# Kernel optimization log

Hardware: AMD Instinct MI355X
Metric: run time of the kernel (lower is better)

## Reference

```python
import jax, jax.numpy as jnp
import numpy as np
import math

N_HEADS = 16
ROPE_BASE = 10000.0


def rotate_half(x):
    x1 = x[..., ::2]
    x2 = x[..., 1::2]
    return jnp.stack((-x2, x1), axis=-1).reshape(x.shape)


def rope_tables(seq_len, head_dim, dtype):
    inv_freq = 1.0 / (ROPE_BASE ** (jnp.arange(0, head_dim, 2, dtype=jnp.float32) / head_dim))
    positions = jnp.arange(seq_len, dtype=jnp.float32)
    freqs = jnp.outer(positions, inv_freq)            # [S, hd/2]
    emb = jnp.concatenate((freqs, freqs), axis=-1)    # [S, hd]  (matches torch cat convention)
    cos = jnp.cos(emb)[None, None, :, :].astype(dtype)
    sin = jnp.sin(emb)[None, None, :, :].astype(dtype)
    return cos, sin


def setup_inputs() -> dict:
    key = jax.random.key(0)
    k1, k2, k3 = jax.random.split(key, 3)
    B, S, D = 2, 2048, 1024
    x = jax.random.normal(k1, (B, S, D), dtype=jnp.float32)
    # causal lower-triangular mask, broadcastable over batch and heads
    mask = jnp.tril(jnp.ones((S, S), dtype=jnp.int32))[None, None, :, :]
    w_qkv = jax.random.normal(k2, (D, 3 * D), dtype=jnp.float32) * 0.02
    w_out = jax.random.normal(k3, (D, D), dtype=jnp.float32) * 0.02
    return {"x": x, "mask": mask, "w_qkv": w_qkv, "w_out": w_out}


def reference(x, mask, w_qkv, w_out):
    B, S, D = x.shape
    H = N_HEADS
    hd = D // H
    qkv = (x @ w_qkv).reshape(B, S, 3, H, hd)
    qkv = jnp.transpose(qkv, (2, 0, 3, 1, 4))         # [3, B, H, S, hd]
    q, k, v = qkv[0], qkv[1], qkv[2]
    cos, sin = rope_tables(S, hd, x.dtype)
    q = q * cos + rotate_half(q) * sin
    k = k * cos + rotate_half(k) * sin
    scale = math.sqrt(hd)
    attn = jnp.einsum("bhsd,bhtd->bhst", q, k) / scale
    attn = jnp.where(mask == 0, -jnp.inf, attn)
    attn = jax.nn.softmax(attn, axis=-1)              # dropout p=0.0 -> identity
    out = jnp.einsum("bhst,bhtd->bhsd", attn, v)
    out = jnp.transpose(out, (0, 2, 1, 3)).reshape(B, S, D)
    return out @ w_out
```

## Files before the change

### kernel.cpp

```cpp
#include <hip/hip_runtime.h>
#include <stdint.h>

typedef unsigned short u16;
typedef __bf16 bf16x8 __attribute__((ext_vector_type(8)));
typedef float f32x4 __attribute__((ext_vector_type(4)));

#define S_LEN 2048
#define NH    16
#define DM    1024
#define N3    3072
#define MROWS 4096

__device__ __forceinline__ float b2f(u16 u) {
  unsigned int v = ((unsigned int)u) << 16;
  return __builtin_bit_cast(float, v);
}
__device__ __forceinline__ u16 f2b(float f) {
  unsigned int v = __builtin_bit_cast(unsigned int, f);
  v += 0x7fffu + ((v >> 16) & 1u);
  return (u16)(v >> 16);
}
__device__ __forceinline__ u16 f2b_trunc(float f) {
  return (u16)(__builtin_bit_cast(unsigned int, f) >> 16);
}
__device__ __forceinline__ bf16x8 ld8(const u16* p) { return *(const bf16x8*)p; }
__device__ __forceinline__ f32x4 mfma16(bf16x8 a, bf16x8 b, f32x4 c) {
  return __builtin_amdgcn_mfma_f32_16x16x32_bf16(a, b, c, 0, 0, 0);
}
__device__ __forceinline__ void glds16(const void* g, void* l) {
  __builtin_amdgcn_global_load_lds(
      (const __attribute__((address_space(1))) unsigned int*)g,
      (__attribute__((address_space(3))) unsigned int*)l, 16, 0, 0);
}
__device__ __forceinline__ int bfish(unsigned int w) {
  unsigned int e = (w >> 7) & 0xffu;
  return (e >= 100u && e <= 134u) ? 1 : 0;
}

__global__ __launch_bounds__(256) void prep_kernel(const void* __restrict__ x,
                                                   const void* __restrict__ wqkv,
                                                   const void* __restrict__ wout,
                                                   u16* __restrict__ xb,
                                                   u16* __restrict__ wqT,
                                                   u16* __restrict__ woT,
                                                   float* __restrict__ cs,
                                                   int* __restrict__ flag) {
  const int bx = blockIdx.x;
  const int t = threadIdx.x;
  if (bx < 2048) {
    __shared__ int cnt;
    if (t == 0) cnt = 0;
    __syncthreads();
    size_t i = (size_t)bx * 256 + t;
    const uint4* xv = (const uint4*)x;
    uint4 probe = xv[i];
    unsigned int wds[4]; *(uint4*)wds = probe;
    atomicAdd(&cnt, bfish(wds[0]) + bfish(wds[1]) + bfish(wds[2]) + bfish(wds[3]));
    __syncthreads();
    const int isbf = cnt > 512;
    if (t == 0) *flag = isbf;
    if (isbf) {
      ((uint4*)xb)[i] = probe;
    } else {
      const float4* xf4 = (const float4*)x;
      uint2* xb2 = (uint2*)xb;
      #pragma unroll
      for (int half = 0; half < 2; ++half) {
        const size_t idx = (size_t)bx * 512 + half * 256 + t;
        const float4 v = xf4[idx];
        u16 pk[4];
        pk[0] = f2b(v.x); pk[1] = f2b(v.y); pk[2] = f2b(v.z); pk[3] = f2b(v.w);
        xb2[idx] = *(const uint2*)pk;
      }
    }
    return;
  }
  if (bx < 2560) {
    int i = (bx - 2048) * 256 + t;
    int s = i >> 6, d = i & 63;
    int f = d & 31;
    float invf = expf(-(float)(2 * f) * (1.0f / 64.0f) * logf(10000.0f));
    float th = (float)s * invf;
    float sv, cv;
    sincosf(th, &sv, &cv);
    cs[i * 2] = cv; cs[i * 2 + 1] = sv;
    return;
  }
  const int wq = bx < 3328;
  const int id = wq ? (bx - 2560) : (bx - 3328);
  const int ncx = wq ? 48 : 16;
  const void* in = wq ? wqkv : wout;
  u16* out = wq ? wqT : woT;
  const int C = wq ? 3072 : 1024;
  const int c0 = (id % ncx) * 64, r0 = (id / ncx) * 64;
  __shared__ int cnt;
  __shared__ u16 L[4096];
  if (t == 0) cnt = 0;
  __syncthreads();
  const unsigned int* wv = (const unsigned int*)in;
  size_t off = (((size_t)id) * 256 + t) & 262143;
  atomicAdd(&cnt, bfish(wv[off]));
  __syncthreads();
  const int fl = cnt > 128;
  if (fl) {
    #pragma unroll
    for (int it = 0; it < 2; ++it) {
      int c = it * 256 + t;
      int rl = c >> 3, cseg = c & 7;
      uint4 v = *(const uint4*)((const u16*)in + (size_t)(r0 + rl) * C + c0 + cseg * 8);
      u16 e[8]; *(uint4*)e = v;
      #pragma unroll
      for (int jj = 0; jj < 8; ++jj) {
        int cl = cseg * 8 + jj;
        L[cl * 64 + (rl ^ (cseg << 3))] = e[jj];
      }
    }
  } else {
    const float* inf_ = (const float*)in;
    #pragma unroll
    for (int it = 0; it < 16; ++it) {
      int c = it * 256 + t;
      int rl = c >> 6, cl = c & 63;
      L[cl * 64 + (rl ^ ((cl >> 3) << 3))] = f2b(inf_[(size_t)(r0 + rl) * C + c0 + cl]);
    }
  }
  __syncthreads();
  #pragma unroll
  for (int it = 0; it < 2; ++it) {
    int c = it * 256 + t;
    int cl = c >> 3, rseg = c & 7;
    uint4 v = *(const uint4*)(L + cl * 64 + (((rseg ^ (cl >> 3)) & 7) << 3));
    *(uint4*)(out + (size_t)(c0 + cl) * 1024 + r0 + rseg * 8) = v;
  }
}


#define PHASE_PRE() do { \
  asm volatile("" ::: "memory"); \
  __builtin_amdgcn_s_barrier(); \
  asm volatile("s_waitcnt lgkmcnt(0)" ::: "memory"); \
  __builtin_amdgcn_sched_barrier(0); \
  __builtin_amdgcn_s_setprio(1); \
} while (0)

#define PHASE_POST() do { \
  __builtin_amdgcn_s_setprio(0); \
  asm volatile("" ::: "memory"); \
  __builtin_amdgcn_s_barrier(); \
} while (0)

#define LOADA(P) \
  _Pragma("unroll") \
  for (int ii = 0; ii < 2; ++ii) { \
    const int row = wr * 128 + ((P) * 2 + ii) * 16 + ln; \
    _Pragma("unroll") \
    for (int kk = 0; kk < 2; ++kk) \
      a[ii][kk] = ld8(Ap + row * 64 + (((kk * 4 + quad) ^ (row & 7)) << 3)); \
  }

#define MFMAQ(P) \
  _Pragma("unroll") \
  for (int ii = 0; ii < 2; ++ii) { \
    _Pragma("unroll") \
    for (int j = 0; j < 4; ++j) { \
      acc[(P) * 2 + ii][j] = mfma16(a[ii][0], b[j][0], acc[(P) * 2 + ii][j]); \
      acc[(P) * 2 + ii][j] = mfma16(a[ii][1], b[j][1], acc[(P) * 2 + ii][j]); \
    } \
  }

__global__ __launch_bounds__(512, 2) void gemm_qkv(const u16* __restrict__ A,
                                                   const u16* __restrict__ Bt,
                                                   u16* __restrict__ Qo,
                                                   u16* __restrict__ Ko,
                                                   u16* __restrict__ Vt,
                                                   const float* __restrict__ cs) {
  __shared__ u16 smem[2][32768];
  const int t = threadIdx.x;
  const int lane = t & 63, wave = t >> 6;
  const int ln = lane & 15, quad = lane >> 4;
  const int wr = wave >> 2, wc = wave & 3;
  const int m0 = blockIdx.x * 256, n0 = blockIdx.y * 256;
  const u16* gA0 = A + (size_t)m0 * 1024;
  const u16* gA1 = A + (size_t)(m0 + 128) * 1024;
  const u16* gB0 = Bt + (size_t)n0 * 1024;
  const u16* gB1 = Bt + (size_t)(n0 + 128) * 1024;
  f32x4 acc[8][4] = {};

  auto stage_half = [&](u16* lds, const u16* g, int k0) {
    #pragma unroll
    for (int it = 0; it < 2; ++it) {
      const int c = it * 512 + t;
      const int row = c >> 3, sg = (c & 7) ^ (row & 7);
      glds16(g + (size_t)row * 1024 + k0 + sg * 8, (char*)lds + c * 16);
    }
  };

  stage_half(&smem[0][0],     gA0, 0);
  stage_half(&smem[0][8192],  gA1, 0);
  stage_half(&smem[0][16384], gB0, 0);
  stage_half(&smem[0][24576], gB1, 0);
  stage_half(&smem[1][16384], gB0, 64);
  stage_half(&smem[1][24576], gB1, 64);
  asm volatile("s_waitcnt vmcnt(4)" ::: "memory");
  __builtin_amdgcn_s_barrier();

  for (int kt = 0; kt < 16; ++kt) {
    const int p = kt & 1;
    u16* Ap = &smem[p][0];
    u16* Bp = &smem[p][16384];
    u16* Aq = &smem[p ^ 1][0];
    const int kA = (kt + 1) * 64, kB = (kt + 2) * 64;
    bf16x8 b[4][2], a[2][2];
    #pragma unroll
    for (int j = 0; j < 4; ++j) {
      const int row = wc * 64 + j * 16 + ln;
      #pragma unroll
      for (int kk = 0; kk < 2; ++kk)
        b[j][kk] = ld8(Bp + row * 64 + (((kk * 4 + quad) ^ (row & 7)) << 3));
    }
    LOADA(0);
    if (kt < 15) stage_half(Aq, gA0, kA);
    PHASE_PRE(); MFMAQ(0); PHASE_POST();
    LOADA(1);
    if (kt < 15) stage_half(Aq + 8192, gA1, kA);
    PHASE_PRE(); MFMAQ(1); PHASE_POST();
    LOADA(2);
    if (kt < 14) stage_half(Bp, gB0, kB);
    PHASE_PRE(); MFMAQ(2); PHASE_POST();
    LOADA(3);
    if (kt < 14) stage_half(Bp + 8192, gB1, kB);
    PHASE_PRE(); MFMAQ(3);
    __builtin_amdgcn_s_setprio(0);
    if (kt < 14) { asm volatile("s_waitcnt vmcnt(4)" ::: "memory"); }
    else         { asm volatile("s_waitcnt vmcnt(0)" ::: "memory"); }
    asm volatile("" ::: "memory");
    __builtin_amdgcn_s_barrier();
  }

  u16* Tl = &smem[0][0];
  const int which = n0 >> 10;
  const int b_ = m0 >> 11;
  const int s0 = m0 & 2047;
  const int h0 = (n0 & 1023) >> 6;

  if (which < 2) {
    const float qs = which ? 1.0f : 0.18033688011112042f;
    const float2* cs2 = (const float2*)cs;
    #pragma unroll
    for (int i = 0; i < 8; ++i) {
      const int slb = wr * 128 + i * 16 + quad * 4;
      #pragma unroll
      for (int j = 0; j < 4; ++j) {
        const int c = wc * 64 + j * 16 + ln;
        const int d = c & 63;
        const float sgn = (d & 1) ? 1.0f : -1.0f;
        #pragma unroll
        for (int r = 0; r < 4; ++r) {
          const int sl = slb + r;
          const float v = acc[i][j][r];
          const float pp = __shfl_xor(v, 1);
          const float2 cv = cs2[(size_t)(s0 + sl) * 64 + d];
          const float val = (v * cv.x + sgn * pp * cv.y) * qs;
          *(u16*)((char*)Tl + sl * 512 + ((((c >> 3) + 4 * (sl & 7)) & 31) << 4)
                  + ((c & 7) << 1)) = f2b(val);
        }
      }
    }
    __syncthreads();
    u16* dst = which ? Ko : Qo;
    #pragma unroll
    for (int it = 0; it < 16; ++it) {
      const int g = it * 512 + t;
      const int c3 = g & 7, sl = (g >> 3) & 255, h = g >> 11;
      const int ch = h * 8 + c3;
      const uint4 vv = *(const uint4*)((const char*)Tl + sl * 512
                        + (((ch + 4 * (sl & 7)) & 31) << 4));
      *(uint4*)(dst + ((size_t)(b_ * NH + h0 + h) * S_LEN + s0 + sl) * 64 + c3 * 8) = vv;
    }
  } else {
    #pragma unroll
    for (int i = 0; i < 8; ++i) {
      const int slb = wr * 128 + i * 16 + quad * 4;
      #pragma unroll
      for (int j = 0; j < 4; ++j) {
        const int c = wc * 64 + j * 16 + ln;
        u16 pk[4];
        #pragma unroll
        for (int r = 0; r < 4; ++r) pk[r] = f2b(acc[i][j][r]);
        *(uint2*)((char*)Tl + c * 512 + ((((slb >> 3) + c) & 31) << 4)
                  + ((slb & 7) << 1)) = *(const uint2*)pk;
      }
    }
    __syncthreads();
    #pragma unroll
    for (int it = 0; it < 16; ++it) {
      const int g = it * 512 + t;
      const int sc = g & 31, cd = g >> 5;
      const int h = cd >> 6, d = cd & 63;
      const uint4 vv = *(const uint4*)((const char*)Tl + cd * 512
                        + (((sc + cd) & 31) << 4));
      *(uint4*)(&Vt[((size_t)((b_ * NH + h0 + h) * 64 + d)) * S_LEN + s0 + sc * 8]) = vv;
    }
  }
}

#undef PHASE_PRE
#undef PHASE_POST
#undef LOADA
#undef MFMAQ

__global__ __launch_bounds__(256) void attn_kernel(const u16* __restrict__ Qb,
                                                   const u16* __restrict__ Kb,
                                                   const u16* __restrict__ Vt,
                                                   u16* __restrict__ Ao) {
  __shared__ u16 smem[20480];
  u16* Kl = smem;
  u16* Vl = smem + 8192;
  u16* Pl = smem + 16384;
  const int t = threadIdx.x;
  const int lane = t & 63, w = t >> 6;
  const int ln = lane & 15, quad = lane >> 4;
  const int i = blockIdx.x;
  const int xcd = i & 7;
  const int j = i >> 3;
  const int bh = (xcd << 2) | (j & 3);
  const int q5 = j >> 2;
  const int g = q5 & 7, s5 = q5 >> 3;
  const int qt = (s5 & 1) ? (31 - ((s5 >> 1) << 3) - g) : (((s5 >> 1) << 3) + g);
  const int q0 = qt * 64;
  const int b = bh >> 4, h = bh & 15;
  const u16* Qbh = Qb + (size_t)bh * (S_LEN * 64);
  const u16* Kbh = Kb + (size_t)bh * (S_LEN * 64);
  const u16* Vtbh = Vt + (size_t)bh * (64 * S_LEN);
  u16* Plw = Pl + w * 1024;
  u16* AoBase = Ao + (size_t)b * S_LEN * DM + h * 64;

  auto stage = [&](int kt, int bufi) {
    u16* kd = Kl + bufi * 4096;
    u16* vd = Vl + bufi * 4096;
    const u16* kg = Kbh + (size_t)kt * 64 * 64;
    const u16* vg = Vtbh + (size_t)kt * 64;
    #pragma unroll
    for (int it = 0; it < 2; ++it) {
      int c = it * 256 + t;
      int row = c >> 3, sg = (c & 7) ^ (row & 7);
      glds16((const char*)kg + ((size_t)row * 64 + sg * 8) * 2,   (char*)kd + c * 16);
      glds16((const char*)vg + ((size_t)row * 2048 + sg * 8) * 2, (char*)vd + c * 16);
    }
  };

  bf16x8 bq[2];
  #pragma unroll
  for (int kk = 0; kk < 2; ++kk)
    bq[kk] = ld8(Qbh + (size_t)(q0 + w * 16 + ln) * 64 + kk * 32 + quad * 8);

  f32x4 o[4] = {};
  float l = 0.f;

  stage(0, 0);
  __syncthreads();

  for (int kt = 0; kt <= qt; ++kt) {
    const int bufi = kt & 1;
    if (kt < qt) stage(kt + 1, bufi ^ 1);
    const u16* Kb_ = Kl + bufi * 4096;
    const u16* Vb_ = Vl + bufi * 4096;

    f32x4 st[4] = {};
    #pragma unroll
    for (int kk = 0; kk < 2; ++kk)
      #pragma unroll
      for (int ct = 0; ct < 4; ++ct) {
        bf16x8 ak = ld8(Kb_ + (ct * 16 + ln) * 64 + (((kk * 4 + quad) ^ (ln & 7)) << 3));
        st[ct] = mfma16(ak, bq[kk], st[ct]);
      }

    const bool diag = (kt == qt);
    #pragma unroll
    for (int ct = 0; ct < 4; ++ct) {
      u16 pk[4];
      #pragma unroll
      for (int r = 0; r < 4; ++r) {
        float p;
        if (diag && (ct * 16 + quad * 4 + r) > (w * 16 + ln)) p = 0.f;
        else p = __builtin_amdgcn_exp2f(st[ct][r]);
        l += p;
        pk[r] = f2b_trunc(p);
      }
      *(uint2*)(Plw + ln * 64 + ((((ct * 2) + (quad >> 1)) ^ (ln & 7)) << 3)
                + ((quad & 1) << 2)) = *(const uint2*)pk;
    }

    #pragma unroll
    for (int k4 = 0; k4 < 2; ++k4) {
      bf16x8 bp = ld8(Plw + ln * 64 + (((k4 * 4 + quad) ^ (ln & 7)) << 3));
      #pragma unroll
      for (int dt = 0; dt < 4; ++dt) {
        bf16x8 av = ld8(Vb_ + (dt * 16 + ln) * 64 + (((k4 * 4 + quad) ^ (ln & 7)) << 3));
        o[dt] = mfma16(av, bp, o[dt]);
      }
    }
    __syncthreads();
  }

  l += __shfl_xor(l, 16);
  l += __shfl_xor(l, 32);
  const float inv = 1.f / l;
  const size_t qrow = (size_t)(q0 + w * 16 + ln) * DM;
  #pragma unroll
  for (int dt = 0; dt < 4; ++dt) {
    u16 pk[4];
    #pragma unroll
    for (int r = 0; r < 4; ++r) pk[r] = f2b(o[dt][r] * inv);
    *(uint2*)(AoBase + qrow + dt * 16 + quad * 4) = *(const uint2*)pk;
  }
}

template <int TM>
__global__ __launch_bounds__(256) void gemm_out_t(const u16* __restrict__ A,
                                                  const u16* __restrict__ Bt,
                                                  void* __restrict__ Out,
                                                  const int* __restrict__ flag) {
  constexpr int MI = TM / 32;
  __shared__ u16 smem[(TM + 128) * 32];
  u16* Al = smem;
  u16* Bl = smem + TM * 32;
  const int t = threadIdx.x;
  const int lane = t & 63, wave = t >> 6;
  const int ln = lane & 15, quad = lane >> 4;
  const int wr = wave >> 1, wc = wave & 1;
  const int m0 = blockIdx.x * TM, n0 = blockIdx.y * 128;
  const int rr = t >> 2;
  const int cb = (t & 3) * 16;
  const char* Ab = (const char*)A;
  const char* Bb = (const char*)Bt;
  f32x4 acc[MI][4] = {};

  for (int k0 = 0; k0 < 1024; k0 += 32) {
    __syncthreads();
    #pragma unroll
    for (int p = 0; p < TM / 64; ++p)
      glds16(Ab + ((size_t)(m0 + p * 64 + rr) * 1024 + k0) * 2 + cb,
             (char*)Al + p * 4096 + t * 16);
    glds16(Bb + ((size_t)(n0 + rr) * 1024 + k0) * 2 + cb,      (char*)Bl + t * 16);
    glds16(Bb + ((size_t)(n0 + 64 + rr) * 1024 + k0) * 2 + cb, (char*)Bl + 4096 + t * 16);
    __syncthreads();
    bf16x8 a[MI], b[4];
    #pragma unroll
    for (int i = 0; i < MI; ++i)
      a[i] = ld8(Al + (wr * (TM / 2) + i * 16 + ln) * 32 + quad * 8);
    #pragma unroll
    for (int j = 0; j < 4; ++j)
      b[j] = ld8(Bl + (wc * 64 + j * 16 + ln) * 32 + quad * 8);
    #pragma unroll
    for (int i = 0; i < MI; ++i)
      #pragma unroll
      for (int j = 0; j < 4; ++j)
        acc[i][j] = mfma16(a[i], b[j], acc[i][j]);
  }

  const int fl = *flag;
  #pragma unroll
  for (int i = 0; i < MI; ++i)
    #pragma unroll
    for (int j = 0; j < 4; ++j)
      #pragma unroll
      for (int r = 0; r < 4; ++r) {
        int m = m0 + wr * (TM / 2) + i * 16 + quad * 4 + r;
        int c = n0 + wc * 64 + j * 16 + ln;
        float v = acc[i][j][r];
        if (fl) ((u16*)Out)[(size_t)m * DM + c] = f2b(v);
        else    ((float*)Out)[(size_t)m * DM + c] = v;
      }
}

extern "C" void kernel_launch(void* const* d_in, const int* in_sizes, int n_in,
                              void* d_out, int out_size, void* d_ws, size_t ws_size,
                              hipStream_t stream) {
  (void)in_sizes; (void)n_in; (void)out_size; (void)ws_size;
  const void* x    = d_in[0];
  const void* wqkv = d_in[2];
  const void* wout = d_in[3];
  char* ws = (char*)d_ws;
  u16*  xb   = (u16*)(ws + 0);
  u16*  Ao   = xb;
  u16*  wqT  = (u16*)(ws + 8388608);
  u16*  woT  = (u16*)(ws + 14680064);
  u16*  Qb   = (u16*)(ws + 16777216);
  u16*  Kb   = (u16*)(ws + 25165824);
  u16*  Vt   = (u16*)(ws + 33554432);
  float* cs  = (float*)(ws + 41943040);
  int*  flag = (int*)(ws + 42991616);

  prep_kernel<<<3584, 256, 0, stream>>>(x, wqkv, wout, xb, wqT, woT, cs, flag);
  gemm_qkv<<<dim3(16, 12), 512, 0, stream>>>(xb, wqT, Qb, Kb, Vt, cs);
  attn_kernel<<<1024, 256, 0, stream>>>(Qb, Kb, Vt, Ao);
  gemm_out_t<64><<<dim3(64, 8), 256, 0, stream>>>(Ao, woT, d_out, flag);
}
```

Baseline: 179.8 us.

## Use 128-row query tiles in attention and K-step 64 in the output GEMM

The attention kernel now runs 512-thread blocks, eight waves, over 128 query rows. Each staged 64-row K/V tile is therefore shared by twice as many query rows, which halves global K/V traffic and per-tile sync overhead. Causal masking becomes a general per-row comparison, so some waves compute fully masked diagonal tiles. The output projection GEMM doubles its K step to 64 and uses XOR-swizzled LDS to cut barrier count and bank conflicts. The cost is half as many attention blocks, which risks load imbalance across CUs and lower occupancy.

```diff
diff --git a/kernel.cpp b/kernel.cpp
--- a/kernel.cpp
+++ b/kernel.cpp
@@ -309,11 +309,11 @@
 #undef LOADA
 #undef MFMAQ
 
-__global__ __launch_bounds__(256) void attn_kernel(const u16* __restrict__ Qb,
+__global__ __launch_bounds__(512) void attn_kernel(const u16* __restrict__ Qb,
                                                    const u16* __restrict__ Kb,
                                                    const u16* __restrict__ Vt,
                                                    u16* __restrict__ Ao) {
-  __shared__ u16 smem[20480];
+  __shared__ u16 smem[24576];
   u16* Kl = smem;
   u16* Vl = smem + 8192;
   u16* Pl = smem + 16384;
@@ -324,10 +324,10 @@
   const int xcd = i & 7;
   const int j = i >> 3;
   const int bh = (xcd << 2) | (j & 3);
-  const int q5 = j >> 2;
-  const int g = q5 & 7, s5 = q5 >> 3;
-  const int qt = (s5 & 1) ? (31 - ((s5 >> 1) << 3) - g) : (((s5 >> 1) << 3) + g);
-  const int q0 = qt * 64;
+  const int idx = j >> 2;
+  const int qtile = (idx & 8) ? (15 - (idx & 7)) : idx;
+  const int q0 = qtile * 128;
+  const int ktmax = 2 * qtile + 1;
   const int b = bh >> 4, h = bh & 15;
   const u16* Qbh = Qb + (size_t)bh * (S_LEN * 64);
   const u16* Kbh = Kb + (size_t)bh * (S_LEN * 64);
@@ -340,13 +340,10 @@
     u16* vd = Vl + bufi * 4096;
     const u16* kg = Kbh + (size_t)kt * 64 * 64;
     const u16* vg = Vtbh + (size_t)kt * 64;
-    #pragma unroll
-    for (int it = 0; it < 2; ++it) {
-      int c = it * 256 + t;
-      int row = c >> 3, sg = (c & 7) ^ (row & 7);
-      glds16((const char*)kg + ((size_t)row * 64 + sg * 8) * 2,   (char*)kd + c * 16);
-      glds16((const char*)vg + ((size_t)row * 2048 + sg * 8) * 2, (char*)vd + c * 16);
-    }
+    const int c = t;
+    const int row = c >> 3, sg = (c & 7) ^ (row & 7);
+    glds16((const char*)kg + ((size_t)row * 64 + sg * 8) * 2,   (char*)kd + c * 16);
+    glds16((const char*)vg + ((size_t)row * 2048 + sg * 8) * 2, (char*)vd + c * 16);
   };
 
   bf16x8 bq[2];
@@ -360,9 +357,9 @@
   stage(0, 0);
   __syncthreads();
 
-  for (int kt = 0; kt <= qt; ++kt) {
+  for (int kt = 0; kt <= ktmax; ++kt) {
     const int bufi = kt & 1;
-    if (kt < qt) stage(kt + 1, bufi ^ 1);
+    if (kt < ktmax) stage(kt + 1, bufi ^ 1);
     const u16* Kb_ = Kl + bufi * 4096;
     const u16* Vb_ = Vl + bufi * 4096;
 
@@ -375,15 +372,14 @@
         st[ct] = mfma16(ak, bq[kk], st[ct]);
       }
 
-    const bool diag = (kt == qt);
+    const int qrel = q0 + w * 16 + ln - kt * 64;
     #pragma unroll
     for (int ct = 0; ct < 4; ++ct) {
       u16 pk[4];
       #pragma unroll
       for (int r = 0; r < 4; ++r) {
-        float p;
-        if (diag && (ct * 16 + quad * 4 + r) > (w * 16 + ln)) p = 0.f;
-        else p = __builtin_amdgcn_exp2f(st[ct][r]);
+        const int lt = ct * 16 + quad * 4 + r;
+        float p = (lt > qrel) ? 0.f : __builtin_amdgcn_exp2f(st[ct][r]);
         l += p;
         pk[r] = f2b_trunc(p);
       }
@@ -422,41 +418,55 @@
                                                   void* __restrict__ Out,
                                                   const int* __restrict__ flag) {
   constexpr int MI = TM / 32;
-  __shared__ u16 smem[(TM + 128) * 32];
+  __shared__ u16 smem[(TM + 128) * 64];
   u16* Al = smem;
-  u16* Bl = smem + TM * 32;
+  u16* Bl = smem + TM * 64;
   const int t = threadIdx.x;
   const int lane = t & 63, wave = t >> 6;
   const int ln = lane & 15, quad = lane >> 4;
   const int wr = wave >> 1, wc = wave & 1;
   const int m0 = blockIdx.x * TM, n0 = blockIdx.y * 128;
-  const int rr = t >> 2;
-  const int cb = (t & 3) * 16;
   const char* Ab = (const char*)A;
   const char* Bb = (const char*)Bt;
   f32x4 acc[MI][4] = {};
 
-  for (int k0 = 0; k0 < 1024; k0 += 32) {
-    __syncthreads();
-    #pragma unroll
-    for (int p = 0; p < TM / 64; ++p)
-      glds16(Ab + ((size_t)(m0 + p * 64 + rr) * 1024 + k0) * 2 + cb,
-             (char*)Al + p * 4096 + t * 16);
-    glds16(Bb + ((size_t)(n0 + rr) * 1024 + k0) * 2 + cb,      (char*)Bl + t * 16);
-    glds16(Bb + ((size_t)(n0 + 64 + rr) * 1024 + k0) * 2 + cb, (char*)Bl + 4096 + t * 16);
-    __syncthreads();
-    bf16x8 a[MI], b[4];
+  for (int k0 = 0; k0 < 1024; k0 += 64) {
+    __syncthreads();
+    #pragma unroll
+    for (int it = 0; it < TM / 32; ++it) {
+      const int c = it * 256 + t;
+      const int row = c >> 3, sg = (c & 7) ^ (row & 7);
+      glds16(Ab + ((size_t)(m0 + row) * 1024 + k0 + sg * 8) * 2, (char*)Al + c * 16);
+    }
+    #pragma unroll
+    for (int it = 0; it < 4; ++it) {
+      const int c = it * 256 + t;
+      const int row = c >> 3, sg = (c & 7) ^ (row & 7);
+      glds16(Bb + ((size_t)(n0 + row) * 1024 + k0 + sg * 8) * 2, (char*)Bl + c * 16);
+    }
+    __syncthreads();
+    bf16x8 a[MI][2], b[4][2];
+    #pragma unroll
+    for (int i = 0; i < MI; ++i) {
+      const int row = wr * (TM / 2) + i * 16 + ln;
+      #pragma unroll
+      for (int kk = 0; kk < 2; ++kk)
+        a[i][kk] = ld8(Al + row * 64 + (((kk * 4 + quad) ^ (row & 7)) << 3));
+    }
+    #pragma unroll
+    for (int j = 0; j < 4; ++j) {
+      const int row = wc * 64 + j * 16 + ln;
+      #pragma unroll
+      for (int kk = 0; kk < 2; ++kk)
+        b[j][kk] = ld8(Bl + row * 64 + (((kk * 4 + quad) ^ (row & 7)) << 3));
+    }
     #pragma unroll
     for (int i = 0; i < MI; ++i)
-      a[i] = ld8(Al + (wr * (TM / 2) + i * 16 + ln) * 32 + quad * 8);
-    #pragma unroll
-    for (int j = 0; j < 4; ++j)
-      b[j] = ld8(Bl + (wc * 64 + j * 16 + ln) * 32 + quad * 8);
-    #pragma unroll
-    for (int i = 0; i < MI; ++i)
-      #pragma unroll
-      for (int j = 0; j < 4; ++j)
-        acc[i][j] = mfma16(a[i], b[j], acc[i][j]);
+      #pragma unroll
+      for (int j = 0; j < 4; ++j) {
+        acc[i][j] = mfma16(a[i][0], b[j][0], acc[i][j]);
+        acc[i][j] = mfma16(a[i][1], b[j][1], acc[i][j]);
+      }
   }
 
   const int fl = *flag;
@@ -494,6 +504,6 @@
 
   prep_kernel<<<3584, 256, 0, stream>>>(x, wqkv, wout, xb, wqT, woT, cs, flag);
   gemm_qkv<<<dim3(16, 12), 512, 0, stream>>>(xb, wqT, Qb, Kb, Vt, cs);
-  attn_kernel<<<1024, 256, 0, stream>>>(Qb, Kb, Vt, Ao);
+  attn_kernel<<<512, 512, 0, stream>>>(Qb, Kb, Vt, Ao);
   gemm_out_t<64><<<dim3(64, 8), 256, 0, stream>>>(Ao, woT, d_out, flag);
 }
```

New measurement: 182.8 us. About the same (+1.7%).
